# Performance work log

Hardware: AMD Instinct MI355X
Metric: run time of the kernel (lower is better)

Reference implementation:

```python
import jax, jax.numpy as jnp
import numpy as np

L, B, H, E, D, S, V, POS = 12, 8, 12, 768, 64, 1024, 50257, 512


def setup_inputs() -> dict:
    key = jax.random.key(0)
    ks = jax.random.split(key, 12)
    r = lambda k, shape: jax.random.normal(k, shape, dtype=jnp.float32) * 0.02
    return {
        "input_ids": jax.random.randint(ks[0], (B, 1), 0, V),
        "cache_position": POS,
        "past_keys": jax.random.normal(ks[1], (L, B, H, S, D), dtype=jnp.float32),
        "past_values": jax.random.normal(ks[2], (L, B, H, S, D), dtype=jnp.float32),
        "wte": r(ks[3], (V, E)),
        "wpe": r(ks[4], (S, E)),
        "ln1_g": jnp.ones((L, E), jnp.float32), "ln1_b": jnp.zeros((L, E), jnp.float32),
        "attn_w": r(ks[5], (L, E, 3 * E)), "attn_b": jnp.zeros((L, 3 * E), jnp.float32),
        "proj_w": r(ks[6], (L, E, E)), "proj_b": jnp.zeros((L, E), jnp.float32),
        "ln2_g": jnp.ones((L, E), jnp.float32), "ln2_b": jnp.zeros((L, E), jnp.float32),
        "fc_w": r(ks[7], (L, E, 4 * E)), "fc_b": jnp.zeros((L, 4 * E), jnp.float32),
        "fcp_w": r(ks[8], (L, 4 * E, E)), "fcp_b": jnp.zeros((L, E), jnp.float32),
        "lnf_g": jnp.ones((E,), jnp.float32), "lnf_b": jnp.zeros((E,), jnp.float32),
    }


def _ln(x, g, b, eps=1e-5):
    m = jnp.mean(x, axis=-1, keepdims=True)
    v = jnp.var(x, axis=-1, keepdims=True)
    return (x - m) * jax.lax.rsqrt(v + eps) * g + b


def reference(input_ids, cache_position, past_keys, past_values, wte, wpe,
              ln1_g, ln1_b, attn_w, attn_b, proj_w, proj_b,
              ln2_g, ln2_b, fc_w, fc_b, fcp_w, fcp_b, lnf_g, lnf_b):
    pos = int(cache_position)          # static decode position
    kv = pos + 1                       # attended cache length (mask==0 inside, -1e4 region sliced off)
    scale = 1.0 / np.sqrt(D).astype(np.float32)
    h = wte[input_ids] + wpe[pos]      # [B,1,E]

    def step(h, xs):
        pk, pv, g1, b1, aw, ab, pw, pb, g2, b2, fw, fb, pw2, pb2 = xs
        x = _ln(h, g1, b1)
        qkv = x @ aw + ab                                  # [B,1,3E]
        q, k, v = jnp.split(qkv, 3, axis=-1)
        q = q.reshape(B, 1, H, D).transpose(0, 2, 1, 3)    # [B,H,1,D]
        k = k.reshape(B, 1, H, D).transpose(0, 2, 1, 3)
        v = v.reshape(B, 1, H, D).transpose(0, 2, 1, 3)
        nk = pk.at[:, :, pos:pos + 1, :].set(k)            # static cache update
        nv = pv.at[:, :, pos:pos + 1, :].set(v)
        ka = nk[:, :, :kv, :]
        va = nv[:, :, :kv, :]
        s = jnp.einsum('bhqd,bhkd->bhqk', q, ka) * scale   # [B,H,1,kv]
        a = jax.nn.softmax(s, axis=-1)
        o = jnp.einsum('bhqk,bhkd->bhqd', a, va)
        o = o.transpose(0, 2, 1, 3).reshape(B, 1, E)
        h = h + o @ pw + pb
        x2 = _ln(h, g2, b2)
        m = jax.nn.gelu(x2 @ fw + fb, approximate=True) @ pw2 + pb2  # gelu_new
        return h + m, (nk, nv)

    h, (new_keys, new_values) = jax.lax.scan(
        step, h,
        (past_keys, past_values, ln1_g, ln1_b, attn_w, attn_b, proj_w, proj_b,
         ln2_g, ln2_b, fc_w, fc_b, fcp_w, fcp_b))
    h = _ln(h, lnf_g, lnf_b)
    logits = h @ wte.T                 # tied lm_head
    return (logits, new_keys, new_values)
```

## Files before the change

### kernel.cpp

```cpp
#include <hip/hip_runtime.h>
#include <hip/hip_bf16.h>

#define LL 12
#define BB 8
#define HH 12
#define EE 768
#define DD 64
#define SS 1024
#define VV 50257
#define E3 2304
#define E4 3072
#define NCH 8
#define CROWS 128

__device__ __forceinline__ float gelu_tanh(float v) {
    float c = 0.7978845608028654f * (v + 0.044715f * v * v * v);
    return 0.5f * v * (1.0f + tanhf(c));
}

__global__ void k_copy(const float4* __restrict__ src, float4* __restrict__ dst, size_t n4) {
    size_t i = (size_t)blockIdx.x * blockDim.x + threadIdx.x;
    size_t stride = (size_t)gridDim.x * blockDim.x;
    for (; i < n4; i += stride) dst[i] = src[i];
}

__global__ void k_pre(const int* __restrict__ ids, const int* __restrict__ posp,
                      const float* __restrict__ wte, const float* __restrict__ wpe,
                      float* __restrict__ hB, float* __restrict__ tmlp,
                      float* __restrict__ qkv, const float* __restrict__ ab0) {
    int blk = blockIdx.x, t = threadIdx.x;
    if (blk < 24) {
        int i = blk * 256 + t;
        int b = i / EE, e = i % EE;
        hB[i] = wte[(size_t)ids[b] * EE + e] + wpe[(size_t)(*posp) * EE + e];
    } else if (blk < 48) {
        int i = (blk - 24) * 256 + t;
        tmlp[i] = 0.f;
    } else {
        int i = (blk - 48) * 256 + t;
        qkv[i] = ab0[i % E3];
    }
}

__device__ __forceinline__ void ln_stats(const float* __restrict__ h1, const float* __restrict__ h2,
                                         float* mean, float* rstd) {
    int t = threadIdx.x, r = t >> 5, l = t & 31;
    float s = 0.f, ss = 0.f;
#pragma unroll
    for (int i = 0; i < 24; i++) {
        int e = l + i * 32;
        float v = h1[r * EE + e] + h2[r * EE + e];
        s += v; ss += v * v;
    }
#pragma unroll
    for (int m = 16; m >= 1; m >>= 1) { s += __shfl_xor(s, m); ss += __shfl_xor(ss, m); }
    if (l == 0) {
        float mu = s * (1.f / EE);
        mean[r] = mu;
        rstd[r] = rsqrtf(ss * (1.f / EE) - mu * mu + 1e-5f);
    }
}

__device__ __forceinline__ void gemm_tile(const float (*xl)[32], const float* __restrict__ W,
                                          float* __restrict__ out, int e0, int c0, int C) {
    int t = threadIdx.x;
    int c = c0 + (t & 63);
    int r2 = (t >> 6) * 2;
    const float* Wp = W + (size_t)e0 * C + c;
    float a0 = 0.f, a1 = 0.f;
#pragma unroll
    for (int e = 0; e < 32; e++) {
        float w = Wp[(size_t)e * C];
        a0 += xl[r2][e] * w;
        a1 += xl[r2 + 1][e] * w;
    }
    atomicAdd(&out[(size_t)r2 * C + c], a0);
    atomicAdd(&out[(size_t)(r2 + 1) * C + c], a1);
}

__global__ void k_ln_gemm(const float* __restrict__ h1, const float* __restrict__ h2,
                          const float* __restrict__ g, const float* __restrict__ bt,
                          const float* __restrict__ W, float* __restrict__ out,
                          int C, int nColBlk,
                          float* __restrict__ hWrite,
                          float* __restrict__ ib, const float* __restrict__ bb, int bC) {
    int nGemm = 24 * nColBlk;
    int blk = blockIdx.x, t = threadIdx.x;
    if (blk >= nGemm) {
        int x = blk - nGemm;
        if (x < 24) { int i = x * 256 + t; hWrite[i] = h1[i] + h2[i]; }
        else { int i = (x - 24) * 256 + t; ib[i] = bb[i % bC]; }
        return;
    }
    int chunk = blk / nColBlk, colblk = blk % nColBlk;
    int e0 = chunk * 32, c0 = colblk * 64;
    __shared__ float xl[8][32];
    __shared__ float mean[8], rstd[8];
    ln_stats(h1, h2, mean, rstd);
    __syncthreads();
    {
        int b = t >> 5, l = t & 31, e = e0 + l;
        xl[b][l] = (h1[b * EE + e] + h2[b * EE + e] - mean[b]) * rstd[b] * g[e] + bt[e];
    }
    __syncthreads();
    gemm_tile(xl, W, out, e0, c0, C);
}

__global__ void k_attn(const float* __restrict__ pk, const float* __restrict__ pv,
                       float* __restrict__ ok, float* __restrict__ ov,
                       const float* __restrict__ qkv,
                       float* __restrict__ pm, float* __restrict__ psum, float* __restrict__ po,
                       const int* __restrict__ posp,
                       float* __restrict__ ib, const float* __restrict__ bb) {
    int blk = blockIdx.x, t = threadIdx.x;
    if (blk >= BB * HH * NCH) {
        int i = (blk - BB * HH * NCH) * 256 + t;
        ib[i] = bb[i % E4];
        return;
    }
    int ch = blk & (NCH - 1), bh = blk >> 3;
    int b = bh / HH, hh = bh % HH;
    int pos = *posp, kv = pos + 1;
    int j0 = ch * CROWS;
    int idx = bh * NCH + ch;
    if (j0 >= kv) { if (t == 0) psum[idx] = 0.f; return; }

    const size_t off = (size_t)bh * SS * DD;
    const float* Kc = pk + off;
    const float* Vc = pv + off;
    const float* qn = qkv + (size_t)b * E3 + hh * DD;
    const float* kn = qn + EE;
    const float* vn = qn + 2 * EE;

    __shared__ float qs[DD], s[CROWS], red[256], bc[2];
    if (t < DD) qs[t] = qn[t];
    __syncthreads();

    int row = t >> 1, half = t & 1;
    int j = j0 + row;
    float sj = 0.f;
    if (j < kv) {
        const float4* s4 = (const float4*)(((j == pos) ? kn : (Kc + (size_t)j * DD)) + half * 32);
#pragma unroll
        for (int i = 0; i < 8; i++) {
            float4 k4 = s4[i];
            sj += k4.x * qs[half * 32 + 4 * i] + k4.y * qs[half * 32 + 4 * i + 1] +
                  k4.z * qs[half * 32 + 4 * i + 2] + k4.w * qs[half * 32 + 4 * i + 3];
        }
    }
    sj += __shfl_xor(sj, 1);
    if (j == pos) {
        float4* dst = (float4*)(ok + off + (size_t)pos * DD + half * 32);
        const float4* sn = (const float4*)(kn + half * 32);
#pragma unroll
        for (int i = 0; i < 8; i++) dst[i] = sn[i];
    }
    if (half == 0) s[row] = (j < kv) ? sj * 0.125f : -INFINITY;
    __syncthreads();

    red[t] = (t < CROWS) ? s[t] : -INFINITY;
    __syncthreads();
    for (int st = 128; st >= 1; st >>= 1) { if (t < st) red[t] = fmaxf(red[t], red[t + st]); __syncthreads(); }
    if (t == 0) bc[0] = red[0];
    __syncthreads();
    float m = bc[0];
    if (t < CROWS) s[t] = __expf(s[t] - m);
    __syncthreads();
    red[t] = (t < CROWS) ? s[t] : 0.f;
    __syncthreads();
    for (int st = 128; st >= 1; st >>= 1) { if (t < st) red[t] += red[t + st]; __syncthreads(); }
    if (t == 0) bc[1] = red[0];

    int d = t & 63, grp = t >> 6;
    float od = 0.f;
    for (int jj = j0 + grp; jj < j0 + CROWS; jj += 4) {
        if (jj == pos) {
            float vv = vn[d];
            ov[off + (size_t)pos * DD + d] = vv;
            od += s[jj - j0] * vv;
        } else if (jj < kv) {
            od += s[jj - j0] * Vc[(size_t)jj * DD + d];
        }
    }
    __syncthreads();
    red[t] = od;
    __syncthreads();
    if (t < 64) {
        float tt = red[t] + red[64 + t] + red[128 + t] + red[192 + t];
        po[(size_t)idx * 64 + t] = tt;
    }
    if (t == 0) { pm[idx] = m; psum[idx] = bc[1]; }
}

__global__ void k_comb_gemm(const float* __restrict__ pm, const float* __restrict__ psum,
                            const float* __restrict__ po,
                            const float* __restrict__ W, float* __restrict__ out,
                            float* __restrict__ ib, const float* __restrict__ bb) {
    const int nGemm = 24 * 12;
    int blk = blockIdx.x, t = threadIdx.x;
    if (blk >= nGemm) {
        int i = (blk - nGemm) * 256 + t;
        ib[i] = bb[i % EE];
        return;
    }
    int chunk = blk / 12, colblk = blk % 12;
    int e0 = chunk * 32, c0 = colblk * 64;
    __shared__ float xl[8][32];
    {
        int b = t >> 5, l = t & 31;
        int e = e0 + l;
        int hh = e >> 6, d = e & 63;
        int bh = b * HH + hh;
        float M = -INFINITY;
#pragma unroll
        for (int ch = 0; ch < NCH; ch++) {
            int idx = bh * NCH + ch;
            if (psum[idx] > 0.f) M = fmaxf(M, pm[idx]);
        }
        float den = 0.f, acc = 0.f;
#pragma unroll
        for (int ch = 0; ch < NCH; ch++) {
            int idx = bh * NCH + ch;
            float ps = psum[idx];
            if (ps > 0.f) {
                float f = __expf(pm[idx] - M);
                den += ps * f;
                acc += po[(size_t)idx * 64 + d] * f;
            }
        }
        xl[b][l] = acc / den;
    }
    __syncthreads();
    gemm_tile(xl, W, out, e0, c0, EE);
}

__global__ void k_gelu_gemm(const float* __restrict__ fc, const float* __restrict__ W,
                            float* __restrict__ out,
                            float* __restrict__ ib, const float* __restrict__ bb) {
    const int nGemm = 96 * 12;
    int blk = blockIdx.x, t = threadIdx.x;
    if (blk >= nGemm) {
        int i = (blk - nGemm) * 256 + t;
        ib[i] = bb[i % E3];
        return;
    }
    int chunk = blk / 12, colblk = blk % 12;
    int e0 = chunk * 32, c0 = colblk * 64;
    __shared__ float xl[8][32];
    {
        int b = t >> 5, l = t & 31;
        xl[b][l] = gelu_tanh(fc[(size_t)b * E4 + e0 + l]);
    }
    __syncthreads();
    gemm_tile(xl, W, out, e0, c0, EE);
}

__global__ void k_logits(const float* __restrict__ h1, const float* __restrict__ h2,
                         const float* __restrict__ g, const float* __restrict__ bt,
                         const float* __restrict__ wte, float* __restrict__ logits) {
    __shared__ float xl[8][768];
    __shared__ float mean[8], rstd[8];
    ln_stats(h1, h2, mean, rstd);
    __syncthreads();
    for (int i = threadIdx.x; i < 8 * 768; i += 256) {
        int b = i / 768, e = i % 768;
        xl[b][e] = (h1[i] + h2[i] - mean[b]) * rstd[b] * g[e] + bt[e];
    }
    __syncthreads();
    int t = threadIdx.x;
    int v = blockIdx.x * 64 + (t >> 2);
    if (v >= VV) return;
    int el = t & 3;
    const float4* w = (const float4*)(wte + (size_t)v * EE);
    float acc[8] = {0, 0, 0, 0, 0, 0, 0, 0};
    for (int i = el; i < 192; i += 4) {
        float4 w4 = w[i];
#pragma unroll
        for (int b = 0; b < 8; b++) {
            float4 xx = ((const float4*)xl[b])[i];
            acc[b] += w4.x * xx.x + w4.y * xx.y + w4.z * xx.z + w4.w * xx.w;
        }
    }
#pragma unroll
    for (int b = 0; b < 8; b++) {
        acc[b] += __shfl_xor(acc[b], 1);
        acc[b] += __shfl_xor(acc[b], 2);
    }
    if (el == 0) {
#pragma unroll
        for (int b = 0; b < 8; b++) logits[(size_t)b * VV + v] = acc[b];
    }
}

extern "C" void kernel_launch(void* const* d_in, const int* in_sizes, int n_in,
                              void* d_out, int out_size, void* d_ws, size_t ws_size,
                              hipStream_t stream) {
    const int* ids = (const int*)d_in[0];
    const int* posp = (const int*)d_in[1];
    const float* past_k = (const float*)d_in[2];
    const float* past_v = (const float*)d_in[3];
    const float* wte = (const float*)d_in[4];
    const float* wpe = (const float*)d_in[5];
    const float* ln1g = (const float*)d_in[6];
    const float* ln1b = (const float*)d_in[7];
    const float* aw = (const float*)d_in[8];
    const float* ab = (const float*)d_in[9];
    const float* pw = (const float*)d_in[10];
    const float* pb = (const float*)d_in[11];
    const float* ln2g = (const float*)d_in[12];
    const float* ln2b = (const float*)d_in[13];
    const float* fw = (const float*)d_in[14];
    const float* fb = (const float*)d_in[15];
    const float* fpw = (const float*)d_in[16];
    const float* fpb = (const float*)d_in[17];
    const float* lnfg = (const float*)d_in[18];
    const float* lnfb = (const float*)d_in[19];

    float* logits = (float*)d_out;
    float* okeys = logits + (size_t)BB * VV;
    float* ovals = okeys + (size_t)LL * BB * HH * SS * DD;

    float* ws = (float*)d_ws;
    float* hB = ws;
    float* hA = hB + BB * EE;
    float* tmlp = hA + BB * EE;
    float* tproj = tmlp + BB * EE;
    float* qkv = tproj + BB * EE;
    float* fcbuf = qkv + BB * E3;
    float* pm = fcbuf + BB * E4;
    float* psum = pm + BB * HH * NCH;
    float* po = psum + BB * HH * NCH;

    const size_t n4 = (size_t)LL * BB * HH * SS * DD / 4;
    k_copy<<<2048, 256, 0, stream>>>((const float4*)past_k, (float4*)okeys, n4);
    k_copy<<<2048, 256, 0, stream>>>((const float4*)past_v, (float4*)ovals, n4);

    k_pre<<<120, 256, 0, stream>>>(ids, posp, wte, wpe, hB, tmlp, qkv, ab);

    for (int l = 0; l < LL; l++) {
        size_t co = (size_t)l * BB * HH * SS * DD;
        k_ln_gemm<<<24 * 36 + 24 + 24, 256, 0, stream>>>(
            hB, tmlp, ln1g + l * EE, ln1b + l * EE, aw + (size_t)l * EE * E3, qkv,
            E3, 36, hA, tproj, pb + (size_t)l * EE, EE);
        k_attn<<<BB * HH * NCH + 96, 256, 0, stream>>>(
            past_k + co, past_v + co, okeys + co, ovals + co,
            qkv, pm, psum, po, posp, fcbuf, fb + (size_t)l * E4);
        k_comb_gemm<<<24 * 12 + 24, 256, 0, stream>>>(
            pm, psum, po, pw + (size_t)l * EE * EE, tproj, tmlp, fpb + (size_t)l * EE);
        k_ln_gemm<<<24 * 48 + 24, 256, 0, stream>>>(
            hA, tproj, ln2g + l * EE, ln2b + l * EE, fw + (size_t)l * EE * E4, fcbuf,
            E4, 48, hB, nullptr, nullptr, 1);
        int extra = (l < LL - 1) ? 72 : 0;
        k_gelu_gemm<<<96 * 12 + extra, 256, 0, stream>>>(
            fcbuf, fpw + (size_t)l * E4 * EE, tmlp, qkv, ab + (size_t)(l + 1) * E3);
    }
    k_logits<<<(VV + 63) / 64, 256, 0, stream>>>(hB, tmlp, lnfg, lnfb, wte, logits);
}
```

Before: 904.8 us.

## Spread KV-cache copy across layer kernels and enlarge GEMM K-chunks

Drops the two standalone full-cache copy kernels. The KV-cache copy is cut into 60 slices, and each of the 60 per-layer launches gets 512 extra blocks that copy one slice, skipping the rows at `pos` that attention writes. The goal is to hide this bandwidth-bound copy behind the latency-bound decode GEMMs and attention. The GEMM reduction chunk grows from 32 to 64, which halves the atomic partial sums. Attention is split into 16 chunks of 64 rows and uses wave-shuffle reductions. The risk is that the copy blocks compete for bandwidth and CUs with the critical-path kernels.

```diff
diff --git a/kernel.cpp b/kernel.cpp
--- a/kernel.cpp
+++ b/kernel.cpp
@@ -10,18 +10,33 @@
 #define VV 50257
 #define E3 2304
 #define E4 3072
-#define NCH 8
-#define CROWS 128
+#define NCH 16
+#define CROWS 64
+#define KCH 64
+
+#define N4HALF 18874368ull
+#define N4TOT  37748736ull
+#define NSLICE 60
+#define W4 ((N4TOT + NSLICE - 1) / NSLICE)
+#define COPYBLK 512
 
 __device__ __forceinline__ float gelu_tanh(float v) {
     float c = 0.7978845608028654f * (v + 0.044715f * v * v * v);
     return 0.5f * v * (1.0f + tanhf(c));
 }
 
-__global__ void k_copy(const float4* __restrict__ src, float4* __restrict__ dst, size_t n4) {
-    size_t i = (size_t)blockIdx.x * blockDim.x + threadIdx.x;
-    size_t stride = (size_t)gridDim.x * blockDim.x;
-    for (; i < n4; i += stride) dst[i] = src[i];
+__device__ __forceinline__ void copy_slice(const float4* __restrict__ kq, const float4* __restrict__ vq,
+                                           float4* __restrict__ ko, float4* __restrict__ vo,
+                                           int pos, int slice, int blkLocal) {
+    size_t base = (size_t)slice * W4;
+    size_t end = base + W4;
+    if (end > N4TOT) end = N4TOT;
+    for (size_t i = base + (size_t)blkLocal * 256 + threadIdx.x; i < end; i += (size_t)COPYBLK * 256) {
+        int row = (int)((i >> 4) & (SS - 1));
+        if (row == pos) continue;
+        if (i < N4HALF) ko[i] = kq[i];
+        else { size_t j = i - N4HALF; vo[j] = vq[j]; }
+    }
 }
 
 __global__ void k_pre(const int* __restrict__ ids, const int* __restrict__ posp,
@@ -61,7 +76,7 @@
     }
 }
 
-__device__ __forceinline__ void gemm_tile(const float (*xl)[32], const float* __restrict__ W,
+__device__ __forceinline__ void gemm_tile(const float (*xl)[KCH], const float* __restrict__ W,
                                           float* __restrict__ out, int e0, int c0, int C) {
     int t = threadIdx.x;
     int c = c0 + (t & 63);
@@ -69,7 +84,7 @@
     const float* Wp = W + (size_t)e0 * C + c;
     float a0 = 0.f, a1 = 0.f;
 #pragma unroll
-    for (int e = 0; e < 32; e++) {
+    for (int e = 0; e < KCH; e++) {
         float w = Wp[(size_t)e * C];
         a0 += xl[r2][e] * w;
         a1 += xl[r2 + 1][e] * w;
@@ -83,51 +98,60 @@
                           const float* __restrict__ W, float* __restrict__ out,
                           int C, int nColBlk,
                           float* __restrict__ hWrite,
-                          float* __restrict__ ib, const float* __restrict__ bb, int bC) {
-    int nGemm = 24 * nColBlk;
-    int blk = blockIdx.x, t = threadIdx.x;
-    if (blk >= nGemm) {
-        int x = blk - nGemm;
-        if (x < 24) { int i = x * 256 + t; hWrite[i] = h1[i] + h2[i]; }
-        else { int i = (x - 24) * 256 + t; ib[i] = bb[i % bC]; }
+                          float* __restrict__ ib, const float* __restrict__ bb, int bC, int nBias,
+                          const float4* __restrict__ kq, const float4* __restrict__ vq,
+                          float4* __restrict__ ko, float4* __restrict__ vo,
+                          const int* __restrict__ posp, int slice) {
+    int nMain = 12 * nColBlk;
+    int blk = blockIdx.x, t = threadIdx.x;
+    if (blk >= nMain) {
+        int x = blk - nMain;
+        if (x < 24) { int i = x * 256 + t; hWrite[i] = h1[i] + h2[i]; return; }
+        x -= 24;
+        if (x < nBias) { int i = x * 256 + t; ib[i] = bb[i % bC]; return; }
+        copy_slice(kq, vq, ko, vo, *posp, slice, x - nBias);
         return;
     }
     int chunk = blk / nColBlk, colblk = blk % nColBlk;
-    int e0 = chunk * 32, c0 = colblk * 64;
-    __shared__ float xl[8][32];
+    int e0 = chunk * KCH, c0 = colblk * 64;
+    __shared__ float xl[8][KCH];
     __shared__ float mean[8], rstd[8];
     ln_stats(h1, h2, mean, rstd);
     __syncthreads();
-    {
-        int b = t >> 5, l = t & 31, e = e0 + l;
+    for (int i = t; i < 8 * KCH; i += 256) {
+        int b = i >> 6, l = i & 63, e = e0 + l;
         xl[b][l] = (h1[b * EE + e] + h2[b * EE + e] - mean[b]) * rstd[b] * g[e] + bt[e];
     }
     __syncthreads();
     gemm_tile(xl, W, out, e0, c0, C);
 }
 
-__global__ void k_attn(const float* __restrict__ pk, const float* __restrict__ pv,
-                       float* __restrict__ ok, float* __restrict__ ov,
+__global__ void k_attn(const float4* __restrict__ kq, const float4* __restrict__ vq,
+                       float4* __restrict__ ko, float4* __restrict__ vo, size_t co,
                        const float* __restrict__ qkv,
                        float* __restrict__ pm, float* __restrict__ psum, float* __restrict__ po,
                        const int* __restrict__ posp,
-                       float* __restrict__ ib, const float* __restrict__ bb) {
-    int blk = blockIdx.x, t = threadIdx.x;
-    if (blk >= BB * HH * NCH) {
-        int i = (blk - BB * HH * NCH) * 256 + t;
-        ib[i] = bb[i % E4];
+                       float* __restrict__ ib, const float* __restrict__ bb, int slice) {
+    const int NMAIN = BB * HH * NCH;
+    int blk = blockIdx.x, t = threadIdx.x;
+    if (blk >= NMAIN) {
+        int x = blk - NMAIN;
+        if (x < 96) { int i = x * 256 + t; ib[i] = bb[i % E4]; return; }
+        copy_slice(kq, vq, ko, vo, *posp, slice, x - 96);
         return;
     }
-    int ch = blk & (NCH - 1), bh = blk >> 3;
+    int ch = blk & (NCH - 1), bh = blk >> 4;
     int b = bh / HH, hh = bh % HH;
     int pos = *posp, kv = pos + 1;
     int j0 = ch * CROWS;
     int idx = bh * NCH + ch;
     if (j0 >= kv) { if (t == 0) psum[idx] = 0.f; return; }
 
-    const size_t off = (size_t)bh * SS * DD;
-    const float* Kc = pk + off;
-    const float* Vc = pv + off;
+    const size_t off = co + (size_t)bh * SS * DD;
+    const float* Kc = (const float*)kq + off;
+    const float* Vc = (const float*)vq + off;
+    float* Ko = (float*)ko + off;
+    float* Vo = (float*)vo + off;
     const float* qn = qkv + (size_t)b * E3 + hh * DD;
     const float* kn = qn + EE;
     const float* vn = qn + 2 * EE;
@@ -136,47 +160,52 @@
     if (t < DD) qs[t] = qn[t];
     __syncthreads();
 
-    int row = t >> 1, half = t & 1;
+    int row = t >> 2, q = t & 3;
     int j = j0 + row;
     float sj = 0.f;
     if (j < kv) {
-        const float4* s4 = (const float4*)(((j == pos) ? kn : (Kc + (size_t)j * DD)) + half * 32);
-#pragma unroll
-        for (int i = 0; i < 8; i++) {
+        const float4* s4 = (const float4*)(((j == pos) ? kn : (Kc + (size_t)j * DD)) + q * 16);
+#pragma unroll
+        for (int i = 0; i < 4; i++) {
             float4 k4 = s4[i];
-            sj += k4.x * qs[half * 32 + 4 * i] + k4.y * qs[half * 32 + 4 * i + 1] +
-                  k4.z * qs[half * 32 + 4 * i + 2] + k4.w * qs[half * 32 + 4 * i + 3];
+            int e = q * 16 + 4 * i;
+            sj += k4.x * qs[e] + k4.y * qs[e + 1] + k4.z * qs[e + 2] + k4.w * qs[e + 3];
         }
     }
     sj += __shfl_xor(sj, 1);
+    sj += __shfl_xor(sj, 2);
     if (j == pos) {
-        float4* dst = (float4*)(ok + off + (size_t)pos * DD + half * 32);
-        const float4* sn = (const float4*)(kn + half * 32);
-#pragma unroll
-        for (int i = 0; i < 8; i++) dst[i] = sn[i];
-    }
-    if (half == 0) s[row] = (j < kv) ? sj * 0.125f : -INFINITY;
-    __syncthreads();
-
-    red[t] = (t < CROWS) ? s[t] : -INFINITY;
-    __syncthreads();
-    for (int st = 128; st >= 1; st >>= 1) { if (t < st) red[t] = fmaxf(red[t], red[t + st]); __syncthreads(); }
-    if (t == 0) bc[0] = red[0];
+        float4* dst = (float4*)(Ko + (size_t)pos * DD + q * 16);
+        const float4* sn = (const float4*)(kn + q * 16);
+#pragma unroll
+        for (int i = 0; i < 4; i++) dst[i] = sn[i];
+    }
+    if (q == 0) s[row] = (j < kv) ? sj * 0.125f : -INFINITY;
+    __syncthreads();
+
+    if (t < 64) {
+        float v = s[t];
+#pragma unroll
+        for (int m = 1; m <= 32; m <<= 1) v = fmaxf(v, __shfl_xor(v, m));
+        if (t == 0) bc[0] = v;
+    }
     __syncthreads();
     float m = bc[0];
-    if (t < CROWS) s[t] = __expf(s[t] - m);
-    __syncthreads();
-    red[t] = (t < CROWS) ? s[t] : 0.f;
-    __syncthreads();
-    for (int st = 128; st >= 1; st >>= 1) { if (t < st) red[t] += red[t + st]; __syncthreads(); }
-    if (t == 0) bc[1] = red[0];
+    if (t < 64) s[t] = __expf(s[t] - m);
+    __syncthreads();
+    if (t < 64) {
+        float p = s[t];
+#pragma unroll
+        for (int mm = 1; mm <= 32; mm <<= 1) p += __shfl_xor(p, mm);
+        if (t == 0) bc[1] = p;
+    }
 
     int d = t & 63, grp = t >> 6;
     float od = 0.f;
     for (int jj = j0 + grp; jj < j0 + CROWS; jj += 4) {
         if (jj == pos) {
             float vv = vn[d];
-            ov[off + (size_t)pos * DD + d] = vv;
+            Vo[(size_t)pos * DD + d] = vv;
             od += s[jj - j0] * vv;
         } else if (jj < kv) {
             od += s[jj - j0] * Vc[(size_t)jj * DD + d];
@@ -195,19 +224,23 @@
 __global__ void k_comb_gemm(const float* __restrict__ pm, const float* __restrict__ psum,
                             const float* __restrict__ po,
                             const float* __restrict__ W, float* __restrict__ out,
-                            float* __restrict__ ib, const float* __restrict__ bb) {
-    const int nGemm = 24 * 12;
-    int blk = blockIdx.x, t = threadIdx.x;
-    if (blk >= nGemm) {
-        int i = (blk - nGemm) * 256 + t;
-        ib[i] = bb[i % EE];
+                            float* __restrict__ ib, const float* __restrict__ bb,
+                            const float4* __restrict__ kq, const float4* __restrict__ vq,
+                            float4* __restrict__ ko, float4* __restrict__ vo,
+                            const int* __restrict__ posp, int slice) {
+    const int nMain = 12 * 12;
+    int blk = blockIdx.x, t = threadIdx.x;
+    if (blk >= nMain) {
+        int x = blk - nMain;
+        if (x < 24) { int i = x * 256 + t; ib[i] = bb[i % EE]; return; }
+        copy_slice(kq, vq, ko, vo, *posp, slice, x - 24);
         return;
     }
     int chunk = blk / 12, colblk = blk % 12;
-    int e0 = chunk * 32, c0 = colblk * 64;
-    __shared__ float xl[8][32];
-    {
-        int b = t >> 5, l = t & 31;
+    int e0 = chunk * KCH, c0 = colblk * 64;
+    __shared__ float xl[8][KCH];
+    for (int i = t; i < 8 * KCH; i += 256) {
+        int b = i >> 6, l = i & 63;
         int e = e0 + l;
         int hh = e >> 6, d = e & 63;
         int bh = b * HH + hh;
@@ -236,19 +269,23 @@
 
 __global__ void k_gelu_gemm(const float* __restrict__ fc, const float* __restrict__ W,
                             float* __restrict__ out,
-                            float* __restrict__ ib, const float* __restrict__ bb) {
-    const int nGemm = 96 * 12;
-    int blk = blockIdx.x, t = threadIdx.x;
-    if (blk >= nGemm) {
-        int i = (blk - nGemm) * 256 + t;
-        ib[i] = bb[i % E3];
+                            float* __restrict__ ib, const float* __restrict__ bb, int nBias,
+                            const float4* __restrict__ kq, const float4* __restrict__ vq,
+                            float4* __restrict__ ko, float4* __restrict__ vo,
+                            const int* __restrict__ posp, int slice) {
+    const int nMain = 48 * 12;
+    int blk = blockIdx.x, t = threadIdx.x;
+    if (blk >= nMain) {
+        int x = blk - nMain;
+        if (x < nBias) { int i = x * 256 + t; ib[i] = bb[i % E3]; return; }
+        copy_slice(kq, vq, ko, vo, *posp, slice, x - nBias);
         return;
     }
     int chunk = blk / 12, colblk = blk % 12;
-    int e0 = chunk * 32, c0 = colblk * 64;
-    __shared__ float xl[8][32];
-    {
-        int b = t >> 5, l = t & 31;
+    int e0 = chunk * KCH, c0 = colblk * 64;
+    __shared__ float xl[8][KCH];
+    for (int i = t; i < 8 * KCH; i += 256) {
+        int b = i >> 6, l = i & 63;
         xl[b][l] = gelu_tanh(fc[(size_t)b * E4 + e0 + l]);
     }
     __syncthreads();
@@ -297,8 +334,8 @@
                               hipStream_t stream) {
     const int* ids = (const int*)d_in[0];
     const int* posp = (const int*)d_in[1];
-    const float* past_k = (const float*)d_in[2];
-    const float* past_v = (const float*)d_in[3];
+    const float4* past_k = (const float4*)d_in[2];
+    const float4* past_v = (const float4*)d_in[3];
     const float* wte = (const float*)d_in[4];
     const float* wpe = (const float*)d_in[5];
     const float* ln1g = (const float*)d_in[6];
@@ -317,8 +354,8 @@
     const float* lnfb = (const float*)d_in[19];
 
     float* logits = (float*)d_out;
-    float* okeys = logits + (size_t)BB * VV;
-    float* ovals = okeys + (size_t)LL * BB * HH * SS * DD;
+    float4* okeys = (float4*)(logits + (size_t)BB * VV);
+    float4* ovals = okeys + N4HALF;
 
     float* ws = (float*)d_ws;
     float* hB = ws;
@@ -331,28 +368,29 @@
     float* psum = pm + BB * HH * NCH;
     float* po = psum + BB * HH * NCH;
 
-    const size_t n4 = (size_t)LL * BB * HH * SS * DD / 4;
-    k_copy<<<2048, 256, 0, stream>>>((const float4*)past_k, (float4*)okeys, n4);
-    k_copy<<<2048, 256, 0, stream>>>((const float4*)past_v, (float4*)ovals, n4);
-
     k_pre<<<120, 256, 0, stream>>>(ids, posp, wte, wpe, hB, tmlp, qkv, ab);
 
     for (int l = 0; l < LL; l++) {
         size_t co = (size_t)l * BB * HH * SS * DD;
-        k_ln_gemm<<<24 * 36 + 24 + 24, 256, 0, stream>>>(
+        int sl = 5 * l;
+        k_ln_gemm<<<12 * 36 + 24 + 24 + COPYBLK, 256, 0, stream>>>(
             hB, tmlp, ln1g + l * EE, ln1b + l * EE, aw + (size_t)l * EE * E3, qkv,
-            E3, 36, hA, tproj, pb + (size_t)l * EE, EE);
-        k_attn<<<BB * HH * NCH + 96, 256, 0, stream>>>(
-            past_k + co, past_v + co, okeys + co, ovals + co,
-            qkv, pm, psum, po, posp, fcbuf, fb + (size_t)l * E4);
-        k_comb_gemm<<<24 * 12 + 24, 256, 0, stream>>>(
-            pm, psum, po, pw + (size_t)l * EE * EE, tproj, tmlp, fpb + (size_t)l * EE);
-        k_ln_gemm<<<24 * 48 + 24, 256, 0, stream>>>(
+            E3, 36, hA, tproj, pb + (size_t)l * EE, EE, 24,
+            past_k, past_v, okeys, ovals, posp, sl + 0);
+        k_attn<<<BB * HH * NCH + 96 + COPYBLK, 256, 0, stream>>>(
+            past_k, past_v, okeys, ovals, co,
+            qkv, pm, psum, po, posp, fcbuf, fb + (size_t)l * E4, sl + 1);
+        k_comb_gemm<<<12 * 12 + 24 + COPYBLK, 256, 0, stream>>>(
+            pm, psum, po, pw + (size_t)l * EE * EE, tproj, tmlp, fpb + (size_t)l * EE,
+            past_k, past_v, okeys, ovals, posp, sl + 2);
+        k_ln_gemm<<<12 * 48 + 24 + 0 + COPYBLK, 256, 0, stream>>>(
             hA, tproj, ln2g + l * EE, ln2b + l * EE, fw + (size_t)l * EE * E4, fcbuf,
-            E4, 48, hB, nullptr, nullptr, 1);
-        int extra = (l < LL - 1) ? 72 : 0;
-        k_gelu_gemm<<<96 * 12 + extra, 256, 0, stream>>>(
-            fcbuf, fpw + (size_t)l * E4 * EE, tmlp, qkv, ab + (size_t)(l + 1) * E3);
+            E4, 48, hB, nullptr, nullptr, 1, 0,
+            past_k, past_v, okeys, ovals, posp, sl + 3);
+        int nBias = (l < LL - 1) ? 72 : 0;
+        k_gelu_gemm<<<48 * 12 + ((l < LL - 1) ? 72 : 0) + COPYBLK, 256, 0, stream>>>(
+            fcbuf, fpw + (size_t)l * E4 * EE, tmlp, qkv, ab + (size_t)(l + 1) * E3, nBias,
+            past_k, past_v, okeys, ovals, posp, sl + 4);
     }
     k_logits<<<(VV + 63) / 64, 256, 0, stream>>>(hB, tmlp, lnfg, lnfb, wte, logits);
 }
```

After: 811.4 us. 1.12x faster.
